# Kernel optimization log

Measured on AMD Instinct MI355X. Metric: run time of the kernel, lower is better.

## Reference

```python
import jax, jax.numpy as jnp
import numpy as np

NODE_DIM = 2
EMB_DIM = 128
SEQ_LEN = 201  # must be odd: depot + N pickups + N deliveries
BATCH = 2048


def _basesin(x, T, fai=0.0):
    return np.sin(2 * np.pi / T * np.abs(np.mod(x, 2 * T) - T) + fai)


def _basecos(x, T, fai=0.0):
    return np.cos(2 * np.pi / T * np.abs(np.mod(x, 2 * T) - T) + fai)


def cyclic_position_encoding_pattern(n_position, emb_dim, mean_pooling=True):
    Td_set = np.linspace(np.power(n_position, 1 / (emb_dim // 2)), n_position,
                         emb_dim // 2, dtype='int')
    x = np.zeros((n_position, emb_dim))
    for i in range(emb_dim):
        Td = Td_set[i // 3 * 3 + 1] if i // 3 * 3 + 1 < emb_dim // 2 else Td_set[-1]
        fai = 0 if i <= emb_dim // 2 else 2 * np.pi * ((-i + emb_dim // 2) / (emb_dim // 2))
        longer = np.arange(0, np.ceil(n_position / Td) * Td, 0.01)
        sel = np.linspace(0, len(longer), n_position, dtype='int', endpoint=False)
        if i % 2 == 1:
            x[:, i] = _basecos(longer, Td, fai)[sel]
        else:
            x[:, i] = _basesin(longer, Td, fai)[sel]
    pattern = x.astype(np.float32)
    pattern_sum = np.zeros_like(pattern)
    arange = np.arange(n_position)
    pooling = [-2, -1, 0, 1, 2] if mean_pooling else [0]
    for i in pooling:
        pattern_sum += pattern[(arange + i + n_position) % n_position]
    pattern = pattern_sum / len(pooling) - pattern.mean(0, keepdims=True)
    return jnp.asarray(pattern)


def setup_inputs() -> dict:
    key = jax.random.key(0)
    kx, kw = jax.random.split(key)
    x = jax.random.normal(kx, (BATCH, SEQ_LEN, NODE_DIM), dtype=jnp.float32)
    # random cyclic permutation per batch: cycle visits all nodes starting at 0
    rng = np.random.default_rng(0)
    r = rng.random((BATCH, SEQ_LEN - 1))
    order = np.concatenate([np.zeros((BATCH, 1), dtype=np.int64),
                            np.argsort(r, axis=1).astype(np.int64) + 1], axis=1)
    nxt = np.roll(order, -1, axis=1)
    sol = np.zeros((BATCH, SEQ_LEN), dtype=np.int64)
    np.put_along_axis(sol, order, nxt, axis=1)
    solutions = jnp.asarray(sol)
    # Linear(node_dim, emb_dim, bias=False), init uniform(-stdv, stdv), stdv=1/sqrt(in)
    stdv = 1.0 / np.sqrt(NODE_DIM)
    W = jax.random.uniform(kw, (EMB_DIM, NODE_DIM), dtype=jnp.float32,
                           minval=-stdv, maxval=stdv)
    pattern = cyclic_position_encoding_pattern(SEQ_LEN, EMB_DIM)
    return {"x": x, "solutions": solutions, "W": W, "pattern": pattern}


def _position_indices(solutions):
    """Pointer-chase over the solution cycle; returns visited_time [B,S] int32
    and top2 [B,S,2] int32 (clac_stacks=True path of the original)."""
    B, S = solutions.shape
    half = S // 2
    arange = jnp.arange(B)
    sol = solutions.astype(jnp.int32)

    visited0 = jnp.zeros((B, S), dtype=jnp.int32)
    pre0 = jnp.zeros((B,), dtype=jnp.int32)
    stacks0 = jnp.full((B, half + 1), -0.01, dtype=jnp.float32).at[:, 0].set(0.0)
    top20 = jnp.zeros((B, S, 2), dtype=jnp.int32)

    def step(carry, i):
        visited, pre, stacks, top2 = carry
        cur = sol[arange, pre]                       # [B] current node
        visited = visited.at[arange, cur].set(i + 1)
        # pickups (0 < cur <= half) push i+1; deliveries (cur > half) pop (-0.01);
        # depot (cur == 0) is a no-op (rewrites stacks[:,0] with itself).
        pos = jnp.where(cur > half, cur - half, cur)
        val = jnp.where(cur == 0, stacks[arange, 0],
                        jnp.where(cur > half, jnp.float32(-0.01),
                                  (i + 1).astype(jnp.float32)))
        stacks = stacks.at[arange, pos].set(val)
        _, idx = jax.lax.top_k(stacks, 2)            # [B,2]
        top2 = top2.at[arange, cur].set(idx.astype(jnp.int32))
        return (visited, cur, stacks, top2), None

    (visited, _, _, top2), _ = jax.lax.scan(
        step, (visited0, pre0, stacks0, top20), jnp.arange(S))
    return visited, top2


def reference(x, solutions, W, pattern):
    visited_time, top2 = _position_indices(solutions)
    S = solutions.shape[1]
    # pos_enc[b, j] = pattern[visited_time[b, j] % S]
    pos_enc = jnp.take(pattern, visited_time % S, axis=0)   # [B,S,D]
    x_embedding = jnp.einsum('bsn,dn->bsd', x, W)           # Linear, no bias
    return x_embedding, pos_enc, visited_time.astype(jnp.int64), top2
```

## Files before the change

kernel.cpp:

```cpp
#include <hip/hip_runtime.h>
#include <stdint.h>

#define B 2048
#define S 201
#define HALF 100
#define D 128
#define BS (B * S)
#define OFF_POS (BS * D)
#define OFF_VT  (2 * OFF_POS)
#define OFF_T2  (OFF_VT + BS)
#define EMB_F4  (BS * (D / 4))

#define NCH 32
#define NEMB 2016
#define NB1 (NCH + NEMB)
#define TPB 256

typedef float  vf4 __attribute__((ext_vector_type(4)));
typedef float  vf2 __attribute__((ext_vector_type(2)));

__global__ __launch_bounds__(TPB) void k1(const float* __restrict__ x,
                                          const int* __restrict__ sol,
                                          const float* __restrict__ W,
                                          float* __restrict__ out,
                                          uint8_t* __restrict__ vt_ws) {
    if (blockIdx.x < NCH) {
        __shared__ uint8_t  s_sol[64 * S];
        __shared__ uint8_t  s_nx [64 * (HALF+1)];
        __shared__ uint8_t  s_pv [64 * (HALF+1)];
        __shared__ uint8_t  s_vis[64 * S];
        __shared__ uint16_t s_t2 [64 * S];
        const int tid = threadIdx.x;
        const int b0  = blockIdx.x * 64;

        for (int idx = tid; idx < 64 * S; idx += TPB) {
            s_sol[idx] = (uint8_t)sol[b0 * S + idx];
            s_vis[idx] = 0;
            s_t2[idx]  = 0;
        }
        __syncthreads();

        if (tid < 64) {
            uint8_t*  sl  = s_sol + tid * S;
            uint8_t*  nx  = s_nx  + tid * (HALF + 1);
            uint8_t*  pv  = s_pv  + tid * (HALF + 1);
            uint8_t*  vis = s_vis + tid * S;
            uint16_t* t2  = s_t2  + tid * S;

            int pre = 0;
            int head = 0, second = 1;
            unsigned long long m0 = 0, m1 = 0;

            for (int i = 0; i < S; ++i) {
                int cur = sl[pre];
                vis[cur] = (uint8_t)(i + 1);
                if (cur != 0) {
                    if (cur <= HALF) {
                        nx[cur]  = (uint8_t)head;
                        pv[head] = (uint8_t)cur;
                        second = head;
                        head   = cur;
                        if (cur < 64) m0 |= 1ull << cur; else m1 |= 1ull << (cur - 64);
                    } else {
                        int q = cur - HALF;
                        bool in = (q < 64) ? ((m0 >> q) & 1ull) : ((m1 >> (q - 64)) & 1ull);
                        if (in) {
                            if (q < 64) m0 &= ~(1ull << q); else m1 &= ~(1ull << (q - 64));
                            if (q == head) {
                                head = second;
                                second = (head == 0) ? 1 : (int)nx[head];
                            } else if (q == second) {
                                int n2 = nx[q];
                                nx[head] = (uint8_t)n2;
                                pv[n2]   = (uint8_t)head;
                                second = n2;
                            } else {
                                int p = pv[q], n2 = nx[q];
                                nx[p]  = (uint8_t)n2;
                                pv[n2] = (uint8_t)p;
                            }
                        }
                    }
                }
                t2[cur] = (uint16_t)(head | (second << 8));
                pre = cur;
            }
        }
        __syncthreads();

        for (int idx = tid; idx < 64 * S; idx += TPB) {
            int v = s_vis[idx];
            out[OFF_VT + b0 * S + idx] = (float)v;
            vt_ws[b0 * S + idx] = (uint8_t)v;
            int t = s_t2[idx];
            vf2 f2 = { (float)(t & 255), (float)(t >> 8) };
            __builtin_nontemporal_store(f2, ((vf2*)(out + OFF_T2)) + b0 * S + idx);
        }
    } else {
        const int d4 = (int)(threadIdx.x & 31);
        const float4* W4 = (const float4*)W;
        float4 w0 = W4[d4 * 2];
        float4 w1 = W4[d4 * 2 + 1];
        const float2* x2 = (const float2*)x;
        vf4* o4 = (vf4*)out;
        const int stride = NEMB * TPB;
        for (int idx4 = (int)(blockIdx.x - NCH) * TPB + (int)threadIdx.x;
             idx4 < EMB_F4; idx4 += stride) {
            float2 xv = x2[idx4 >> 5];
            vf4 o;
            o.x = xv.x * w0.x + xv.y * w0.y;
            o.y = xv.x * w0.z + xv.y * w0.w;
            o.z = xv.x * w1.x + xv.y * w1.y;
            o.w = xv.x * w1.z + xv.y * w1.w;
            __builtin_nontemporal_store(o, &o4[idx4]);
        }
    }
}

__global__ __launch_bounds__(TPB) void k2(const float* __restrict__ pattern,
                                          const uint8_t* __restrict__ vt_ws,
                                          float* __restrict__ out) {
    const vf4* p4 = (const vf4*)pattern;
    vf4* o4 = (vf4*)(out + OFF_POS);
    const int stride = (int)(gridDim.x * blockDim.x);
    for (int idx4 = (int)(blockIdx.x * blockDim.x + threadIdx.x);
         idx4 < EMB_F4; idx4 += stride) {
        int vt = vt_ws[idx4 >> 5];
        int row = (vt >= S) ? (vt - S) : vt;
        vf4 v = p4[row * 32 + (idx4 & 31)];
        __builtin_nontemporal_store(v, &o4[idx4]);
    }
}

extern "C" void kernel_launch(void* const* d_in, const int* in_sizes, int n_in,
                              void* d_out, int out_size, void* d_ws, size_t ws_size,
                              hipStream_t stream) {
    const float* x       = (const float*)d_in[0];
    const int*   sol     = (const int*)d_in[1];
    const float* W       = (const float*)d_in[2];
    const float* pattern = (const float*)d_in[3];
    float* out = (float*)d_out;
    uint8_t* vt_ws = (uint8_t*)d_ws;

    hipLaunchKernelGGL(k1, dim3(NB1), dim3(TPB), 0, stream, x, sol, W, out, vt_ws);
    hipLaunchKernelGGL(k2, dim3(2048), dim3(TPB), 0, stream, pattern, vt_ws, out);
}
```

Before: 465.3 us.

## Split sequential scan into tiny kernel and fuse all output writes into one kernel

The serial per-batch stack simulation now runs alone in a 32-block kernel that writes visited times and top2 indices to workspace. A second kernel writes the embedding, the positional encoding gather, and the visited/top2 float outputs in one grid-stride pass. Before, the embedding work was co-scheduled with the scan blocks. The intent is to merge the write-heavy passes and use regular stores instead of nontemporal ones. The trade-off is that the serial scan is no longer overlapped with the embedding writes and now sits on the critical path before any output streaming starts.

Result: slower. 506.1 us (+8.8%).

```diff
diff --git a/kernel.cpp b/kernel.cpp
--- a/kernel.cpp
+++ b/kernel.cpp
@@ -11,124 +11,122 @@
 #define OFF_T2  (OFF_VT + BS)
 #define EMB_F4  (BS * (D / 4))
 
-#define NCH 32
-#define NEMB 2016
-#define NB1 (NCH + NEMB)
 #define TPB 256
+#define NB_B 4096
 
-typedef float  vf4 __attribute__((ext_vector_type(4)));
-typedef float  vf2 __attribute__((ext_vector_type(2)));
+typedef float vf4 __attribute__((ext_vector_type(4)));
 
-__global__ __launch_bounds__(TPB) void k1(const float* __restrict__ x,
-                                          const int* __restrict__ sol,
-                                          const float* __restrict__ W,
-                                          float* __restrict__ out,
-                                          uint8_t* __restrict__ vt_ws) {
-    if (blockIdx.x < NCH) {
-        __shared__ uint8_t  s_sol[64 * S];
-        __shared__ uint8_t  s_nx [64 * (HALF+1)];
-        __shared__ uint8_t  s_pv [64 * (HALF+1)];
-        __shared__ uint8_t  s_vis[64 * S];
-        __shared__ uint16_t s_t2 [64 * S];
-        const int tid = threadIdx.x;
-        const int b0  = blockIdx.x * 64;
+__global__ __launch_bounds__(TPB) void kA(const int* __restrict__ sol,
+                                          uint8_t* __restrict__ ws) {
+    __shared__ uint8_t  s_sol[64 * S];
+    __shared__ uint8_t  s_nx [64 * (HALF + 1)];
+    __shared__ uint8_t  s_pv [64 * (HALF + 1)];
+    __shared__ uint8_t  s_vis[64 * S];
+    __shared__ uint16_t s_t2 [64 * S];
+    const int tid = threadIdx.x;
+    const int b0  = blockIdx.x * 64;
 
-        for (int idx = tid; idx < 64 * S; idx += TPB) {
-            s_sol[idx] = (uint8_t)sol[b0 * S + idx];
-            s_vis[idx] = 0;
-            s_t2[idx]  = 0;
-        }
-        __syncthreads();
+    for (int idx = tid; idx < 64 * S; idx += TPB) {
+        s_sol[idx] = (uint8_t)sol[b0 * S + idx];
+        s_vis[idx] = 0;
+        s_t2[idx]  = 0;
+    }
+    __syncthreads();
 
-        if (tid < 64) {
-            uint8_t*  sl  = s_sol + tid * S;
-            uint8_t*  nx  = s_nx  + tid * (HALF + 1);
-            uint8_t*  pv  = s_pv  + tid * (HALF + 1);
-            uint8_t*  vis = s_vis + tid * S;
-            uint16_t* t2  = s_t2  + tid * S;
+    if (tid < 64) {
+        uint8_t*  sl  = s_sol + tid * S;
+        uint8_t*  nx  = s_nx  + tid * (HALF + 1);
+        uint8_t*  pv  = s_pv  + tid * (HALF + 1);
+        uint8_t*  vis = s_vis + tid * S;
+        uint16_t* t2  = s_t2  + tid * S;
 
-            int pre = 0;
-            int head = 0, second = 1;
-            unsigned long long m0 = 0, m1 = 0;
+        int pre = 0;
+        int head = 0, second = 1;
+        unsigned long long m0 = 0, m1 = 0;
 
-            for (int i = 0; i < S; ++i) {
-                int cur = sl[pre];
-                vis[cur] = (uint8_t)(i + 1);
-                if (cur != 0) {
-                    if (cur <= HALF) {
-                        nx[cur]  = (uint8_t)head;
-                        pv[head] = (uint8_t)cur;
-                        second = head;
-                        head   = cur;
-                        if (cur < 64) m0 |= 1ull << cur; else m1 |= 1ull << (cur - 64);
-                    } else {
-                        int q = cur - HALF;
-                        bool in = (q < 64) ? ((m0 >> q) & 1ull) : ((m1 >> (q - 64)) & 1ull);
-                        if (in) {
-                            if (q < 64) m0 &= ~(1ull << q); else m1 &= ~(1ull << (q - 64));
-                            if (q == head) {
-                                head = second;
-                                second = (head == 0) ? 1 : (int)nx[head];
-                            } else if (q == second) {
-                                int n2 = nx[q];
-                                nx[head] = (uint8_t)n2;
-                                pv[n2]   = (uint8_t)head;
-                                second = n2;
-                            } else {
-                                int p = pv[q], n2 = nx[q];
-                                nx[p]  = (uint8_t)n2;
-                                pv[n2] = (uint8_t)p;
-                            }
+        for (int i = 0; i < S; ++i) {
+            int cur = sl[pre];
+            vis[cur] = (uint8_t)(i + 1);
+            if (cur != 0) {
+                if (cur <= HALF) {
+                    nx[cur]  = (uint8_t)head;
+                    pv[head] = (uint8_t)cur;
+                    second = head;
+                    head   = cur;
+                    if (cur < 64) m0 |= 1ull << cur; else m1 |= 1ull << (cur - 64);
+                } else {
+                    int q = cur - HALF;
+                    bool in = (q < 64) ? ((m0 >> q) & 1ull) : ((m1 >> (q - 64)) & 1ull);
+                    if (in) {
+                        if (q < 64) m0 &= ~(1ull << q); else m1 &= ~(1ull << (q - 64));
+                        if (q == head) {
+                            head = second;
+                            second = (head == 0) ? 1 : (int)nx[head];
+                        } else if (q == second) {
+                            int n2 = nx[q];
+                            nx[head] = (uint8_t)n2;
+                            pv[n2]   = (uint8_t)head;
+                            second = n2;
+                        } else {
+                            int p = pv[q], n2 = nx[q];
+                            nx[p]  = (uint8_t)n2;
+                            pv[n2] = (uint8_t)p;
                         }
                     }
                 }
-                t2[cur] = (uint16_t)(head | (second << 8));
-                pre = cur;
             }
+            t2[cur] = (uint16_t)(head | (second << 8));
+            pre = cur;
         }
-        __syncthreads();
+    }
+    __syncthreads();
 
-        for (int idx = tid; idx < 64 * S; idx += TPB) {
-            int v = s_vis[idx];
-            out[OFF_VT + b0 * S + idx] = (float)v;
-            vt_ws[b0 * S + idx] = (uint8_t)v;
-            int t = s_t2[idx];
-            vf2 f2 = { (float)(t & 255), (float)(t >> 8) };
-            __builtin_nontemporal_store(f2, ((vf2*)(out + OFF_T2)) + b0 * S + idx);
-        }
-    } else {
-        const int d4 = (int)(threadIdx.x & 31);
-        const float4* W4 = (const float4*)W;
-        float4 w0 = W4[d4 * 2];
-        float4 w1 = W4[d4 * 2 + 1];
-        const float2* x2 = (const float2*)x;
-        vf4* o4 = (vf4*)out;
-        const int stride = NEMB * TPB;
-        for (int idx4 = (int)(blockIdx.x - NCH) * TPB + (int)threadIdx.x;
-             idx4 < EMB_F4; idx4 += stride) {
-            float2 xv = x2[idx4 >> 5];
-            vf4 o;
-            o.x = xv.x * w0.x + xv.y * w0.y;
-            o.y = xv.x * w0.z + xv.y * w0.w;
-            o.z = xv.x * w1.x + xv.y * w1.y;
-            o.w = xv.x * w1.z + xv.y * w1.w;
-            __builtin_nontemporal_store(o, &o4[idx4]);
-        }
+    uint16_t* t2_ws = (uint16_t*)(ws + BS);
+    for (int idx = tid; idx < 64 * S; idx += TPB) {
+        ws[b0 * S + idx]    = s_vis[idx];
+        t2_ws[b0 * S + idx] = s_t2[idx];
     }
 }
 
-__global__ __launch_bounds__(TPB) void k2(const float* __restrict__ pattern,
-                                          const uint8_t* __restrict__ vt_ws,
+__global__ __launch_bounds__(TPB) void kB(const float* __restrict__ x,
+                                          const float* __restrict__ W,
+                                          const float* __restrict__ pattern,
+                                          const uint8_t* __restrict__ ws,
                                           float* __restrict__ out) {
+    const int tid   = (int)(blockIdx.x * TPB + threadIdx.x);
+    const int nthr  = NB_B * TPB;
+
+    const int d4 = tid & 31;
+    const float4* W4 = (const float4*)W;
+    float4 w0 = W4[d4 * 2];
+    float4 w1 = W4[d4 * 2 + 1];
+
+    const float2* x2 = (const float2*)x;
     const vf4* p4 = (const vf4*)pattern;
-    vf4* o4 = (vf4*)(out + OFF_POS);
-    const int stride = (int)(gridDim.x * blockDim.x);
-    for (int idx4 = (int)(blockIdx.x * blockDim.x + threadIdx.x);
-         idx4 < EMB_F4; idx4 += stride) {
-        int vt = vt_ws[idx4 >> 5];
+    vf4* oe = (vf4*)out;
+    vf4* op = (vf4*)(out + OFF_POS);
+
+    for (int idx4 = tid; idx4 < EMB_F4; idx4 += nthr) {
+        int bs = idx4 >> 5;
+        float2 xv = x2[bs];
+        vf4 o;
+        o.x = xv.x * w0.x + xv.y * w0.y;
+        o.y = xv.x * w0.z + xv.y * w0.w;
+        o.z = xv.x * w1.x + xv.y * w1.y;
+        o.w = xv.x * w1.z + xv.y * w1.w;
+        oe[idx4] = o;
+        int vt = ws[bs];
         int row = (vt >= S) ? (vt - S) : vt;
-        vf4 v = p4[row * 32 + (idx4 & 31)];
-        __builtin_nontemporal_store(v, &o4[idx4]);
+        op[idx4] = p4[row * 32 + d4];
+    }
+
+    const uint16_t* t2_ws = (const uint16_t*)(ws + BS);
+    float*  ovt = out + OFF_VT;
+    float2* ot2 = (float2*)(out + OFF_T2);
+    for (int idx = tid; idx < BS; idx += nthr) {
+        ovt[idx] = (float)ws[idx];
+        int t = t2_ws[idx];
+        ot2[idx] = make_float2((float)(t & 255), (float)(t >> 8));
     }
 }
 
@@ -140,8 +138,8 @@
     const float* W       = (const float*)d_in[2];
     const float* pattern = (const float*)d_in[3];
     float* out = (float*)d_out;
-    uint8_t* vt_ws = (uint8_t*)d_ws;
+    uint8_t* ws = (uint8_t*)d_ws;
 
-    hipLaunchKernelGGL(k1, dim3(NB1), dim3(TPB), 0, stream, x, sol, W, out, vt_ws);
-    hipLaunchKernelGGL(k2, dim3(2048), dim3(TPB), 0, stream, pattern, vt_ws, out);
+    hipLaunchKernelGGL(kA, dim3(32), dim3(TPB), 0, stream, sol, ws);
+    hipLaunchKernelGGL(kB, dim3(NB_B), dim3(TPB), 0, stream, x, W, pattern, ws, out);
 }
```
